# Performance work log

Measured on AMD Instinct MI355X. Metric: run time of the kernel, lower is better.

The kernel has to match this reference:

```python
import jax, jax.numpy as jnp
import numpy as np

N_NODES = 100000
E_MAIN = 1600000   # '_E' edges
E_ACC = 200000     # 'account' edges
D = 128            # dim_in == dim_out
FE = 4             # edge feature width (hard-coded in source)


def setup_inputs() -> dict:
    key = jax.random.key(0)
    ks = jax.random.split(key, 14)
    inp = {
        "feats": jax.random.normal(ks[0], (N_NODES, D), jnp.float32),
        "edge_feats": jax.random.normal(ks[1], (E_MAIN, FE), jnp.float32),
        "src_E": jax.random.randint(ks[2], (E_MAIN,), 0, N_NODES),
        "dst_E": jax.random.randint(ks[3], (E_MAIN,), 0, N_NODES),
        "src_acc": jax.random.randint(ks[4], (E_ACC,), 0, N_NODES),
        "dst_acc": jax.random.randint(ks[5], (E_ACC,), 0, N_NODES),
        "W_skip": jax.random.normal(ks[6], (D, D), jnp.float32) * 0.05,
        "b_skip": jnp.zeros((D,), jnp.float32),
        "W_msg": jax.random.normal(ks[7], (D, D), jnp.float32) * 0.05,
        "b_msg": jnp.zeros((D,), jnp.float32),
        "W_edge": jax.random.normal(ks[8], (D, FE), jnp.float32) * 0.5,
        "b_edge": jax.random.normal(ks[9], (D,), jnp.float32) * 0.1,
        "W_att": jax.random.normal(ks[10], (1, FE), jnp.float32) * 0.5,
        "b_att": jax.random.normal(ks[11], (1,), jnp.float32) * 0.1,
    }
    return inp


def reference(feats, edge_feats, src_E, dst_E, src_acc, dst_acc,
              W_skip, b_skip, W_msg, b_msg, W_edge, b_edge, W_att, b_att):
    n = feats.shape[0]
    # symmetric-ish degree norm from '_E' source rows (matches self.norm)
    deg = jax.ops.segment_sum(jnp.ones(src_E.shape[0], feats.dtype), src_E,
                              num_segments=n)
    deg_safe = jnp.where(deg > 0, deg, 1.0)
    norm = jnp.where(deg > 0, deg_safe ** -0.5, 0.0)  # [N]
    h = feats * norm[:, None]                         # srcdata['h'] == dstdata['h']

    def messages(ef, s, d):
        # per-edge: sigmoid attention * src + transformed edge feat + dst
        att = jax.nn.sigmoid(ef @ W_att.T + b_att)    # [E,1]
        tr = ef @ W_edge.T + b_edge                   # [E,D]
        return att * h[s] + tr + h[d]                 # [E,D]

    agg = jax.ops.segment_sum(messages(edge_feats, src_E, dst_E), dst_E,
                              num_segments=n)
    # 'account' etype gets zero edge features (as in source)
    ef_acc = jnp.zeros((src_acc.shape[0], edge_feats.shape[1]), feats.dtype)
    agg = agg + jax.ops.segment_sum(messages(ef_acc, src_acc, dst_acc), dst_acc,
                                    num_segments=n)

    rst = agg * norm[:, None]
    return rst @ W_msg.T + b_msg + (feats @ W_skip.T + b_skip)
```

## Files before the change

### kernel.cpp

```cpp
#include <hip/hip_runtime.h>
#include <hip/hip_bf16.h>

#define NN 100000
#define NP 100096
#define EM 1600000
#define EA 200000
#define ET (EM + EA)
#define SB 98

#define HC 128
#define CNT_CHUNK 14063
#define DEG_CHUNK 12500
#define PITCHW 25024
#define PITCHB 100096

#define OFF_NORM 0
#define OFF_CNT  (NN)
#define OFF_CUR  (2*NN)
#define OFF_BSUM (3*NN)
#define OFF_WB   (3*NN + 128)
#define OFF_REC  (OFF_WB + 16384)
#define OFF_FB   (OFF_REC + 4*ET)
#define OFF_RB   (OFF_FB + 64*NP)
#define OFF_RANK (OFF_RB + 64*NP)

#define UNP_LO(u) __uint_as_float((u) << 16)
#define UNP_HI(u) __uint_as_float((u) & 0xFFFF0000u)

typedef __attribute__((ext_vector_type(8))) short bf16x8;
typedef __attribute__((ext_vector_type(4))) float f32x4;

static __device__ __forceinline__ unsigned pack_bf16x2(float a, float b) {
  union { __hip_bfloat162 v; unsigned u; } cv;
  cv.v = __float22bfloat162_rn(make_float2(a, b));
  return cv.u;
}

__global__ __launch_bounds__(1024) void k_hist(
    const int* __restrict__ srcE, const int* __restrict__ dstE,
    const int* __restrict__ dstA, const float* __restrict__ feats,
    unsigned* __restrict__ featsb,
    unsigned* __restrict__ hist8w, unsigned* __restrict__ deg8w,
    unsigned short* __restrict__ rank16) {
  __shared__ unsigned h[PITCHW];
  int tid = threadIdx.x;
  int bid = blockIdx.x;

  for (int i = bid * 1024 + tid; i < NP * 64; i += 2 * HC * 1024) {
    if (i < NN * 64) {
      float2 f = ((const float2*)feats)[i];
      featsb[i] = pack_bf16x2(f.x, f.y);
    } else {
      featsb[i] = 0u;
    }
  }

  for (int i = tid; i < PITCHW; i += 1024) h[i] = 0u;
  __syncthreads();
  if (bid < HC) {
    int c = bid;
    int e1 = c * CNT_CHUNK + CNT_CHUNK; if (e1 > ET) e1 = ET;
    for (int e = c * CNT_CHUNK + tid; e < e1; e += 1024) {
      int d = (e < EM) ? dstE[e] : dstA[e - EM];
      unsigned sh = 8u * (unsigned)(d & 3);
      unsigned old = atomicAdd(&h[d >> 2], 1u << sh);
      unsigned lr = (old >> sh) & 255u;
      rank16[e] = (unsigned short)(((unsigned)c << 9) | lr);
    }
    __syncthreads();
    unsigned* dst = hist8w + (size_t)c * PITCHW;
    for (int i = tid; i < PITCHW; i += 1024) dst[i] = h[i];
  } else {
    int c = bid - HC;
    int e1 = c * DEG_CHUNK + DEG_CHUNK;
    for (int e = c * DEG_CHUNK + tid; e < e1; e += 1024) {
      int s = srcE[e];
      atomicAdd(&h[s >> 2], 1u << (8u * (unsigned)(s & 3)));
    }
    __syncthreads();
    unsigned* dst = deg8w + (size_t)c * PITCHW;
    for (int i = tid; i < PITCHW; i += 1024) dst[i] = h[i];
  }
}

__global__ __launch_bounds__(256) void k_merge_wt(
    unsigned char* __restrict__ hist8, const unsigned char* __restrict__ deg8,
    unsigned* __restrict__ cnt, float* __restrict__ norm,
    const float* __restrict__ Wmsg, const float* __restrict__ Wskip,
    unsigned* __restrict__ Wb) {
  int i = blockIdx.x * 256 + threadIdx.x;
  if (i < NN) {
    unsigned t = 0;
    for (int c = 0; c < HC; ++c) {
      unsigned char* p = hist8 + (size_t)c * PITCHB + i;
      unsigned b = *p;
      *p = (unsigned char)t;
      t += b;
    }
    cnt[i] = t;
    unsigned dg = 0;
    for (int c = 0; c < HC; ++c) dg += deg8[(size_t)c * PITCHB + i];
    norm[i] = dg ? rsqrtf((float)dg) : 0.0f;
  }
  if (i < 16384) {
    int j = i >> 7, kk = i & 127;
    float a, b;
    if (kk < 64) {
      a = Wmsg[j * 128 + 2 * kk];
      b = Wmsg[j * 128 + 2 * kk + 1];
    } else {
      a = Wskip[j * 128 + 2 * kk - 128];
      b = Wskip[j * 128 + 2 * kk - 127];
    }
    Wb[j * 128 + kk] = pack_bf16x2(a, b);
  }
}

__global__ __launch_bounds__(1024) void k_scan1(const unsigned* __restrict__ cnt,
                                                int* __restrict__ bsum) {
  __shared__ int ws16[16];
  int tid = threadIdx.x, lane = tid & 63, wid = tid >> 6;
  int i = blockIdx.x * 1024 + tid;
  int v = (i < NN) ? (int)cnt[i] : 0;
#pragma unroll
  for (int s = 1; s < 64; s <<= 1) v += __shfl_xor(v, s, 64);
  if (lane == 0) ws16[wid] = v;
  __syncthreads();
  if (tid == 0) {
    int a = 0;
#pragma unroll
    for (int w = 0; w < 16; ++w) a += ws16[w];
    bsum[blockIdx.x] = a;
  }
}

__global__ __launch_bounds__(64) void k_scan2(int* __restrict__ bsum) {
  int lane = threadIdx.x;
  int v0 = (lane < SB) ? bsum[lane] : 0;
  int v1 = (64 + lane < SB) ? bsum[64 + lane] : 0;
  int x0 = v0, x1 = v1;
#pragma unroll
  for (int s = 1; s < 64; s <<= 1) {
    int y = __shfl_up(x0, s, 64); if (lane >= s) x0 += y;
  }
#pragma unroll
  for (int s = 1; s < 64; s <<= 1) {
    int y = __shfl_up(x1, s, 64); if (lane >= s) x1 += y;
  }
  int t0 = __shfl(x0, 63, 64);
  if (lane < SB) bsum[lane] = x0 - v0;
  if (64 + lane < SB) bsum[64 + lane] = t0 + x1 - v1;
}

__global__ __launch_bounds__(1024) void k_scan3(const unsigned* __restrict__ cnt,
                                                const int* __restrict__ bsum,
                                                int* __restrict__ cursor) {
  __shared__ int ws16[16];
  int tid = threadIdx.x, lane = tid & 63, wid = tid >> 6;
  int i = blockIdx.x * 1024 + tid;
  int v = (i < NN) ? (int)cnt[i] : 0;
  int x = v;
#pragma unroll
  for (int s = 1; s < 64; s <<= 1) {
    int y = __shfl_up(x, s, 64); if (lane >= s) x += y;
  }
  if (lane == 63) ws16[wid] = x;
  __syncthreads();
  if (tid == 0) {
    int a = bsum[blockIdx.x];
#pragma unroll
    for (int w = 0; w < 16; ++w) { int t = ws16[w]; ws16[w] = a; a += t; }
  }
  __syncthreads();
  if (i < NN) cursor[i] = ws16[wid] + x - v;
}

__global__ __launch_bounds__(256) void k_fill(
    const int* __restrict__ srcE, const int* __restrict__ dstE,
    const int* __restrict__ srcA, const int* __restrict__ dstA,
    const float* __restrict__ ef, const float* __restrict__ Watt,
    const float* __restrict__ batt, const float* __restrict__ norm,
    const int* __restrict__ cursor, const unsigned char* __restrict__ hist8,
    const unsigned short* __restrict__ rank16,
    uint4* __restrict__ rec) {
  int e = blockIdx.x * 256 + threadIdx.x;
  if (e >= ET) return;
  int s, d;
  float att;
  float4 f;
  if (e < EM) {
    s = srcE[e]; d = dstE[e];
    f = ((const float4*)ef)[e];
    float z = f.x * Watt[0] + f.y * Watt[1] + f.z * Watt[2] + f.w * Watt[3] + batt[0];
    att = 1.0f / (1.0f + __expf(-z));
  } else {
    int ea = e - EM;
    s = srcA[ea]; d = dstA[ea];
    f = make_float4(0.f, 0.f, 0.f, 0.f);
    att = 1.0f / (1.0f + __expf(-batt[0]));
  }
  float c = att * norm[s];
  unsigned rr = rank16[e];
  int slot = cursor[d] + (int)hist8[(size_t)(rr >> 9) * PITCHB + d]
           + (int)(rr & 511u);
  rec[slot] = make_uint4((unsigned)s, __float_as_uint(c),
                         pack_bf16x2(f.x, f.y), pack_bf16x2(f.z, f.w));
}

__global__ __launch_bounds__(256) void k_pull(
    const float* __restrict__ feats, const unsigned* __restrict__ featsb,
    const unsigned* __restrict__ cnt, const int* __restrict__ cursor,
    const float* __restrict__ norm, const uint4* __restrict__ rec,
    const float* __restrict__ Wedge, const float* __restrict__ bedge,
    unsigned* __restrict__ rstb) {
  int lane = threadIdx.x & 63, wid = threadIdx.x >> 6;
  int n = blockIdx.x * 4 + wid;
  if (n >= NP) return;
  if (n >= NN) { rstb[n * 64 + lane] = 0u; return; }

  int beg = __builtin_amdgcn_readfirstlane(cursor[n]);
  int len = __builtin_amdgcn_readfirstlane((int)cnt[n]);
  int end = beg + len;
  float2 acc = make_float2(0.f, 0.f);
  float4 efa = make_float4(0.f, 0.f, 0.f, 0.f);
  int e = beg;
  for (; e + 8 <= end; e += 8) {
    uint4 r0 = rec[e+0], r1 = rec[e+1], r2 = rec[e+2], r3 = rec[e+3];
    uint4 r4 = rec[e+4], r5 = rec[e+5], r6 = rec[e+6], r7 = rec[e+7];
    unsigned u0 = featsb[r0.x * 64 + lane];
    unsigned u1 = featsb[r1.x * 64 + lane];
    unsigned u2 = featsb[r2.x * 64 + lane];
    unsigned u3 = featsb[r3.x * 64 + lane];
    unsigned u4 = featsb[r4.x * 64 + lane];
    unsigned u5 = featsb[r5.x * 64 + lane];
    unsigned u6 = featsb[r6.x * 64 + lane];
    unsigned u7 = featsb[r7.x * 64 + lane];
    float c0 = __uint_as_float(r0.y), c1 = __uint_as_float(r1.y);
    float c2 = __uint_as_float(r2.y), c3 = __uint_as_float(r3.y);
    float c4 = __uint_as_float(r4.y), c5 = __uint_as_float(r5.y);
    float c6 = __uint_as_float(r6.y), c7 = __uint_as_float(r7.y);
    acc.x += c0 * UNP_LO(u0) + c1 * UNP_LO(u1) + c2 * UNP_LO(u2) + c3 * UNP_LO(u3)
           + c4 * UNP_LO(u4) + c5 * UNP_LO(u5) + c6 * UNP_LO(u6) + c7 * UNP_LO(u7);
    acc.y += c0 * UNP_HI(u0) + c1 * UNP_HI(u1) + c2 * UNP_HI(u2) + c3 * UNP_HI(u3)
           + c4 * UNP_HI(u4) + c5 * UNP_HI(u5) + c6 * UNP_HI(u6) + c7 * UNP_HI(u7);
    efa.x += UNP_LO(r0.z) + UNP_LO(r1.z) + UNP_LO(r2.z) + UNP_LO(r3.z)
           + UNP_LO(r4.z) + UNP_LO(r5.z) + UNP_LO(r6.z) + UNP_LO(r7.z);
    efa.y += UNP_HI(r0.z) + UNP_HI(r1.z) + UNP_HI(r2.z) + UNP_HI(r3.z)
           + UNP_HI(r4.z) + UNP_HI(r5.z) + UNP_HI(r6.z) + UNP_HI(r7.z);
    efa.z += UNP_LO(r0.w) + UNP_LO(r1.w) + UNP_LO(r2.w) + UNP_LO(r3.w)
           + UNP_LO(r4.w) + UNP_LO(r5.w) + UNP_LO(r6.w) + UNP_LO(r7.w);
    efa.w += UNP_HI(r0.w) + UNP_HI(r1.w) + UNP_HI(r2.w) + UNP_HI(r3.w)
           + UNP_HI(r4.w) + UNP_HI(r5.w) + UNP_HI(r6.w) + UNP_HI(r7.w);
  }
  for (; e < end; ++e) {
    uint4 r = rec[e];
    unsigned u = featsb[r.x * 64 + lane];
    float c = __uint_as_float(r.y);
    acc.x += c * UNP_LO(u);
    acc.y += c * UNP_HI(u);
    efa.x += UNP_LO(r.z); efa.y += UNP_HI(r.z);
    efa.z += UNP_LO(r.w); efa.w += UNP_HI(r.w);
  }
  float flen = (float)len;
  float nm = norm[n];
  float2 f = ((const float2*)feats)[n * 64 + lane];
  float4 wa = ((const float4*)Wedge)[2 * lane + 0];
  float4 wb = ((const float4*)Wedge)[2 * lane + 1];
  float2 be = ((const float2*)bedge)[lane];
  float tx = wa.x * efa.x + wa.y * efa.y + wa.z * efa.z + wa.w * efa.w;
  float ty = wb.x * efa.x + wb.y * efa.y + wb.z * efa.z + wb.w * efa.w;
  float rx = (acc.x + tx + flen * (be.x + nm * f.x)) * nm;
  float ry = (acc.y + ty + flen * (be.y + nm * f.y)) * nm;
  rstb[n * 64 + lane] = pack_bf16x2(rx, ry);
}

__global__ __launch_bounds__(256) void k_gemm(
    const unsigned* __restrict__ rstb, const unsigned* __restrict__ featsb,
    const unsigned* __restrict__ Wb,
    const float* __restrict__ bmsg, const float* __restrict__ bskip,
    float* __restrict__ out) {
  int lane = threadIdx.x & 63, wid = threadIdx.x >> 6;
  int quad = lane >> 4, l15 = lane & 15;
  int rowt = blockIdx.x * 128 + wid * 32;
  int m0 = rowt + l15;
  int m1 = m0 + 16;

  f32x4 acc0[8], acc1[8];
#pragma unroll
  for (int ct = 0; ct < 8; ++ct) {
    acc0[ct] = (f32x4){0.f, 0.f, 0.f, 0.f};
    acc1[ct] = (f32x4){0.f, 0.f, 0.f, 0.f};
  }

#pragma unroll
  for (int ks = 0; ks < 8; ++ks) {
    int kb = ks * 32;
    const unsigned* Xsrc = (kb < 128) ? rstb : featsb;
    int off = ((kb & 127) >> 1) + quad * 4;
    bf16x8 a0 = *(const bf16x8*)(Xsrc + m0 * 64 + off);
    bf16x8 a1 = *(const bf16x8*)(Xsrc + m1 * 64 + off);
#pragma unroll
    for (int ct = 0; ct < 8; ++ct) {
      int j = ct * 16 + l15;
      bf16x8 b = *(const bf16x8*)(Wb + j * 128 + (kb >> 1) + quad * 4);
      acc0[ct] = __builtin_amdgcn_mfma_f32_16x16x32_bf16(a0, b, acc0[ct], 0, 0, 0);
      acc1[ct] = __builtin_amdgcn_mfma_f32_16x16x32_bf16(a1, b, acc1[ct], 0, 0, 0);
    }
  }

#pragma unroll
  for (int ct = 0; ct < 8; ++ct) {
    int col = ct * 16 + l15;
    float bia = bmsg[col] + bskip[col];
#pragma unroll
    for (int r = 0; r < 4; ++r) {
      int row0 = rowt + quad * 4 + r;
      if (row0 < NN) out[row0 * 128 + col] = acc0[ct][r] + bia;
      int row1 = row0 + 16;
      if (row1 < NN) out[row1 * 128 + col] = acc1[ct][r] + bia;
    }
  }
}

extern "C" void kernel_launch(void* const* d_in, const int* in_sizes, int n_in,
                              void* d_out, int out_size, void* d_ws, size_t ws_size,
                              hipStream_t stream) {
  const float* feats  = (const float*)d_in[0];
  const float* ef     = (const float*)d_in[1];
  const int*   srcE   = (const int*)d_in[2];
  const int*   dstE   = (const int*)d_in[3];
  const int*   srcA   = (const int*)d_in[4];
  const int*   dstA   = (const int*)d_in[5];
  const float* Wskip  = (const float*)d_in[6];
  const float* bskip  = (const float*)d_in[7];
  const float* Wmsg   = (const float*)d_in[8];
  const float* bmsg   = (const float*)d_in[9];
  const float* Wedge  = (const float*)d_in[10];
  const float* bedge  = (const float*)d_in[11];
  const float* Watt   = (const float*)d_in[12];
  const float* batt   = (const float*)d_in[13];
  float* out = (float*)d_out;
  float* ws  = (float*)d_ws;

  float*          norm   = ws + OFF_NORM;
  unsigned*       cnt    = (unsigned*)(ws + OFF_CNT);
  int*            cursor = (int*)(ws + OFF_CUR);
  int*            bsum   = (int*)(ws + OFF_BSUM);
  unsigned*       Wb     = (unsigned*)(ws + OFF_WB);
  uint4*          rec    = (uint4*)(ws + OFF_REC);
  unsigned*       featsb = (unsigned*)(ws + OFF_FB);
  unsigned*       rstb   = (unsigned*)(ws + OFF_RB);
  unsigned short* rank16 = (unsigned short*)(ws + OFF_RANK);

  unsigned*       hist8w = rstb;
  unsigned*       deg8w  = rstb + (size_t)HC * PITCHW;
  unsigned char*  hist8b = (unsigned char*)hist8w;
  unsigned char*  deg8b  = (unsigned char*)deg8w;

  k_hist<<<2 * HC, 1024, 0, stream>>>(srcE, dstE, dstA, feats, featsb,
                                      hist8w, deg8w, rank16);
  k_merge_wt<<<(NN + 255) / 256, 256, 0, stream>>>(hist8b, deg8b, cnt, norm,
                                                   Wmsg, Wskip, Wb);
  k_scan1<<<SB, 1024, 0, stream>>>(cnt, bsum);
  k_scan2<<<1, 64, 0, stream>>>(bsum);
  k_scan3<<<SB, 1024, 0, stream>>>(cnt, bsum, cursor);
  k_fill<<<(ET + 255) / 256, 256, 0, stream>>>(srcE, dstE, srcA, dstA, ef, Watt,
                                               batt, norm, cursor, hist8b,
                                               rank16, rec);
  k_pull<<<NP / 4, 256, 0, stream>>>(feats, featsb, cnt, cursor, norm,
                                     rec, Wedge, bedge, rstb);
  k_gemm<<<NP / 128, 256, 0, stream>>>(rstb, featsb, Wb, bmsg, bskip, out);
}
```

Baseline: 374.4 us.

## Fuse pull aggregation and output GEMM into one kernel via LDS tile

Merges the per-node gather/aggregate kernel and the MFMA GEMM into a single kernel: each 256-thread block aggregates 64 nodes (16 per wave, sequentially) into a bf16 LDS tile, then runs the GEMM on that tile plus the bf16 features. This removes the global round trip of the intermediate rst buffer and one launch, and reads the destination features from the bf16 copy instead of fp32. The trade-off is fewer blocks (NP/64 instead of NP/4), each wave processing 16 nodes serially, which lowers memory-level parallelism for the latency-bound gather. The self term also loses precision from using bf16 feats.

New measurement: 415.2 us. 10.9% more time.

```diff
diff --git a/kernel.cpp b/kernel.cpp
--- a/kernel.cpp
+++ b/kernel.cpp
@@ -21,8 +21,8 @@
 #define OFF_WB   (3*NN + 128)
 #define OFF_REC  (OFF_WB + 16384)
 #define OFF_FB   (OFF_REC + 4*ET)
-#define OFF_RB   (OFF_FB + 64*NP)
-#define OFF_RANK (OFF_RB + 64*NP)
+#define OFF_HIST (OFF_FB + 64*NP)
+#define OFF_RANK (OFF_HIST + 64*NP)
 
 #define UNP_LO(u) __uint_as_float((u) << 16)
 #define UNP_HI(u) __uint_as_float((u) & 0xFFFF0000u)
@@ -207,104 +207,109 @@
                          pack_bf16x2(f.x, f.y), pack_bf16x2(f.z, f.w));
 }
 
-__global__ __launch_bounds__(256) void k_pull(
-    const float* __restrict__ feats, const unsigned* __restrict__ featsb,
+__global__ __launch_bounds__(256, 4) void k_pullgemm(
+    const unsigned* __restrict__ featsb,
     const unsigned* __restrict__ cnt, const int* __restrict__ cursor,
     const float* __restrict__ norm, const uint4* __restrict__ rec,
     const float* __restrict__ Wedge, const float* __restrict__ bedge,
-    unsigned* __restrict__ rstb) {
+    const unsigned* __restrict__ Wb,
+    const float* __restrict__ bmsg, const float* __restrict__ bskip,
+    float* __restrict__ out) {
+  __shared__ unsigned lA[64 * 68];
   int lane = threadIdx.x & 63, wid = threadIdx.x >> 6;
-  int n = blockIdx.x * 4 + wid;
-  if (n >= NP) return;
-  if (n >= NN) { rstb[n * 64 + lane] = 0u; return; }
-
-  int beg = __builtin_amdgcn_readfirstlane(cursor[n]);
-  int len = __builtin_amdgcn_readfirstlane((int)cnt[n]);
-  int end = beg + len;
-  float2 acc = make_float2(0.f, 0.f);
-  float4 efa = make_float4(0.f, 0.f, 0.f, 0.f);
-  int e = beg;
-  for (; e + 8 <= end; e += 8) {
-    uint4 r0 = rec[e+0], r1 = rec[e+1], r2 = rec[e+2], r3 = rec[e+3];
-    uint4 r4 = rec[e+4], r5 = rec[e+5], r6 = rec[e+6], r7 = rec[e+7];
-    unsigned u0 = featsb[r0.x * 64 + lane];
-    unsigned u1 = featsb[r1.x * 64 + lane];
-    unsigned u2 = featsb[r2.x * 64 + lane];
-    unsigned u3 = featsb[r3.x * 64 + lane];
-    unsigned u4 = featsb[r4.x * 64 + lane];
-    unsigned u5 = featsb[r5.x * 64 + lane];
-    unsigned u6 = featsb[r6.x * 64 + lane];
-    unsigned u7 = featsb[r7.x * 64 + lane];
-    float c0 = __uint_as_float(r0.y), c1 = __uint_as_float(r1.y);
-    float c2 = __uint_as_float(r2.y), c3 = __uint_as_float(r3.y);
-    float c4 = __uint_as_float(r4.y), c5 = __uint_as_float(r5.y);
-    float c6 = __uint_as_float(r6.y), c7 = __uint_as_float(r7.y);
-    acc.x += c0 * UNP_LO(u0) + c1 * UNP_LO(u1) + c2 * UNP_LO(u2) + c3 * UNP_LO(u3)
-           + c4 * UNP_LO(u4) + c5 * UNP_LO(u5) + c6 * UNP_LO(u6) + c7 * UNP_LO(u7);
-    acc.y += c0 * UNP_HI(u0) + c1 * UNP_HI(u1) + c2 * UNP_HI(u2) + c3 * UNP_HI(u3)
-           + c4 * UNP_HI(u4) + c5 * UNP_HI(u5) + c6 * UNP_HI(u6) + c7 * UNP_HI(u7);
-    efa.x += UNP_LO(r0.z) + UNP_LO(r1.z) + UNP_LO(r2.z) + UNP_LO(r3.z)
-           + UNP_LO(r4.z) + UNP_LO(r5.z) + UNP_LO(r6.z) + UNP_LO(r7.z);
-    efa.y += UNP_HI(r0.z) + UNP_HI(r1.z) + UNP_HI(r2.z) + UNP_HI(r3.z)
-           + UNP_HI(r4.z) + UNP_HI(r5.z) + UNP_HI(r6.z) + UNP_HI(r7.z);
-    efa.z += UNP_LO(r0.w) + UNP_LO(r1.w) + UNP_LO(r2.w) + UNP_LO(r3.w)
-           + UNP_LO(r4.w) + UNP_LO(r5.w) + UNP_LO(r6.w) + UNP_LO(r7.w);
-    efa.w += UNP_HI(r0.w) + UNP_HI(r1.w) + UNP_HI(r2.w) + UNP_HI(r3.w)
-           + UNP_HI(r4.w) + UNP_HI(r5.w) + UNP_HI(r6.w) + UNP_HI(r7.w);
-  }
-  for (; e < end; ++e) {
-    uint4 r = rec[e];
-    unsigned u = featsb[r.x * 64 + lane];
-    float c = __uint_as_float(r.y);
-    acc.x += c * UNP_LO(u);
-    acc.y += c * UNP_HI(u);
-    efa.x += UNP_LO(r.z); efa.y += UNP_HI(r.z);
-    efa.z += UNP_LO(r.w); efa.w += UNP_HI(r.w);
-  }
-  float flen = (float)len;
-  float nm = norm[n];
-  float2 f = ((const float2*)feats)[n * 64 + lane];
+  int rowt = blockIdx.x * 64;
+
   float4 wa = ((const float4*)Wedge)[2 * lane + 0];
   float4 wb = ((const float4*)Wedge)[2 * lane + 1];
   float2 be = ((const float2*)bedge)[lane];
-  float tx = wa.x * efa.x + wa.y * efa.y + wa.z * efa.z + wa.w * efa.w;
-  float ty = wb.x * efa.x + wb.y * efa.y + wb.z * efa.z + wb.w * efa.w;
-  float rx = (acc.x + tx + flen * (be.x + nm * f.x)) * nm;
-  float ry = (acc.y + ty + flen * (be.y + nm * f.y)) * nm;
-  rstb[n * 64 + lane] = pack_bf16x2(rx, ry);
-}
-
-__global__ __launch_bounds__(256) void k_gemm(
-    const unsigned* __restrict__ rstb, const unsigned* __restrict__ featsb,
-    const unsigned* __restrict__ Wb,
-    const float* __restrict__ bmsg, const float* __restrict__ bskip,
-    float* __restrict__ out) {
-  int lane = threadIdx.x & 63, wid = threadIdx.x >> 6;
+
+  for (int i = 0; i < 16; ++i) {
+    int rloc = wid * 16 + i;
+    int n = rowt + rloc;
+    float rx = 0.f, ry = 0.f;
+    if (n < NN) {
+      int beg = __builtin_amdgcn_readfirstlane(cursor[n]);
+      int len = __builtin_amdgcn_readfirstlane((int)cnt[n]);
+      int end = beg + len;
+      float2 acc = make_float2(0.f, 0.f);
+      float4 efa = make_float4(0.f, 0.f, 0.f, 0.f);
+      int e = beg;
+      for (; e + 8 <= end; e += 8) {
+        uint4 r0 = rec[e+0], r1 = rec[e+1], r2 = rec[e+2], r3 = rec[e+3];
+        uint4 r4 = rec[e+4], r5 = rec[e+5], r6 = rec[e+6], r7 = rec[e+7];
+        unsigned u0 = featsb[r0.x * 64 + lane];
+        unsigned u1 = featsb[r1.x * 64 + lane];
+        unsigned u2 = featsb[r2.x * 64 + lane];
+        unsigned u3 = featsb[r3.x * 64 + lane];
+        unsigned u4 = featsb[r4.x * 64 + lane];
+        unsigned u5 = featsb[r5.x * 64 + lane];
+        unsigned u6 = featsb[r6.x * 64 + lane];
+        unsigned u7 = featsb[r7.x * 64 + lane];
+        float c0 = __uint_as_float(r0.y), c1 = __uint_as_float(r1.y);
+        float c2 = __uint_as_float(r2.y), c3 = __uint_as_float(r3.y);
+        float c4 = __uint_as_float(r4.y), c5 = __uint_as_float(r5.y);
+        float c6 = __uint_as_float(r6.y), c7 = __uint_as_float(r7.y);
+        acc.x += c0 * UNP_LO(u0) + c1 * UNP_LO(u1) + c2 * UNP_LO(u2)
+               + c3 * UNP_LO(u3) + c4 * UNP_LO(u4) + c5 * UNP_LO(u5)
+               + c6 * UNP_LO(u6) + c7 * UNP_LO(u7);
+        acc.y += c0 * UNP_HI(u0) + c1 * UNP_HI(u1) + c2 * UNP_HI(u2)
+               + c3 * UNP_HI(u3) + c4 * UNP_HI(u4) + c5 * UNP_HI(u5)
+               + c6 * UNP_HI(u6) + c7 * UNP_HI(u7);
+        efa.x += UNP_LO(r0.z) + UNP_LO(r1.z) + UNP_LO(r2.z) + UNP_LO(r3.z)
+               + UNP_LO(r4.z) + UNP_LO(r5.z) + UNP_LO(r6.z) + UNP_LO(r7.z);
+        efa.y += UNP_HI(r0.z) + UNP_HI(r1.z) + UNP_HI(r2.z) + UNP_HI(r3.z)
+               + UNP_HI(r4.z) + UNP_HI(r5.z) + UNP_HI(r6.z) + UNP_HI(r7.z);
+        efa.z += UNP_LO(r0.w) + UNP_LO(r1.w) + UNP_LO(r2.w) + UNP_LO(r3.w)
+               + UNP_LO(r4.w) + UNP_LO(r5.w) + UNP_LO(r6.w) + UNP_LO(r7.w);
+        efa.w += UNP_HI(r0.w) + UNP_HI(r1.w) + UNP_HI(r2.w) + UNP_HI(r3.w)
+               + UNP_HI(r4.w) + UNP_HI(r5.w) + UNP_HI(r6.w) + UNP_HI(r7.w);
+      }
+      for (; e < end; ++e) {
+        uint4 r = rec[e];
+        unsigned u = featsb[r.x * 64 + lane];
+        float c = __uint_as_float(r.y);
+        acc.x += c * UNP_LO(u);
+        acc.y += c * UNP_HI(u);
+        efa.x += UNP_LO(r.z); efa.y += UNP_HI(r.z);
+        efa.z += UNP_LO(r.w); efa.w += UNP_HI(r.w);
+      }
+      float flen = (float)len;
+      float nm = norm[n];
+      unsigned ud = featsb[n * 64 + lane];
+      float fx = UNP_LO(ud), fy = UNP_HI(ud);
+      float tx = wa.x * efa.x + wa.y * efa.y + wa.z * efa.z + wa.w * efa.w;
+      float ty = wb.x * efa.x + wb.y * efa.y + wb.z * efa.z + wb.w * efa.w;
+      rx = (acc.x + tx + flen * (be.x + nm * fx)) * nm;
+      ry = (acc.y + ty + flen * (be.y + nm * fy)) * nm;
+    }
+    lA[rloc * 68 + lane] = pack_bf16x2(rx, ry);
+  }
+  __syncthreads();
+
   int quad = lane >> 4, l15 = lane & 15;
-  int rowt = blockIdx.x * 128 + wid * 32;
-  int m0 = rowt + l15;
-  int m1 = m0 + 16;
-
-  f32x4 acc0[8], acc1[8];
-#pragma unroll
-  for (int ct = 0; ct < 8; ++ct) {
-    acc0[ct] = (f32x4){0.f, 0.f, 0.f, 0.f};
-    acc1[ct] = (f32x4){0.f, 0.f, 0.f, 0.f};
-  }
+  int rloc0 = wid * 16 + l15;
+  int m0 = rowt + rloc0;
+
+  f32x4 acc0[8];
+#pragma unroll
+  for (int ct = 0; ct < 8; ++ct) acc0[ct] = (f32x4){0.f, 0.f, 0.f, 0.f};
 
 #pragma unroll
   for (int ks = 0; ks < 8; ++ks) {
     int kb = ks * 32;
-    const unsigned* Xsrc = (kb < 128) ? rstb : featsb;
-    int off = ((kb & 127) >> 1) + quad * 4;
-    bf16x8 a0 = *(const bf16x8*)(Xsrc + m0 * 64 + off);
-    bf16x8 a1 = *(const bf16x8*)(Xsrc + m1 * 64 + off);
+    bf16x8 a0;
+    if (ks < 4) {
+      int off = ks * 16 + quad * 4;
+      a0 = *(const bf16x8*)(&lA[rloc0 * 68 + off]);
+    } else {
+      int off = ((kb & 127) >> 1) + quad * 4;
+      a0 = *(const bf16x8*)(featsb + (size_t)m0 * 64 + off);
+    }
 #pragma unroll
     for (int ct = 0; ct < 8; ++ct) {
       int j = ct * 16 + l15;
       bf16x8 b = *(const bf16x8*)(Wb + j * 128 + (kb >> 1) + quad * 4);
       acc0[ct] = __builtin_amdgcn_mfma_f32_16x16x32_bf16(a0, b, acc0[ct], 0, 0, 0);
-      acc1[ct] = __builtin_amdgcn_mfma_f32_16x16x32_bf16(a1, b, acc1[ct], 0, 0, 0);
     }
   }
 
@@ -314,10 +319,8 @@
     float bia = bmsg[col] + bskip[col];
 #pragma unroll
     for (int r = 0; r < 4; ++r) {
-      int row0 = rowt + quad * 4 + r;
+      int row0 = rowt + wid * 16 + quad * 4 + r;
       if (row0 < NN) out[row0 * 128 + col] = acc0[ct][r] + bia;
-      int row1 = row0 + 16;
-      if (row1 < NN) out[row1 * 128 + col] = acc1[ct][r] + bia;
     }
   }
 }
@@ -349,11 +352,10 @@
   unsigned*       Wb     = (unsigned*)(ws + OFF_WB);
   uint4*          rec    = (uint4*)(ws + OFF_REC);
   unsigned*       featsb = (unsigned*)(ws + OFF_FB);
-  unsigned*       rstb   = (unsigned*)(ws + OFF_RB);
   unsigned short* rank16 = (unsigned short*)(ws + OFF_RANK);
 
-  unsigned*       hist8w = rstb;
-  unsigned*       deg8w  = rstb + (size_t)HC * PITCHW;
+  unsigned*       hist8w = (unsigned*)(ws + OFF_HIST);
+  unsigned*       deg8w  = hist8w + (size_t)HC * PITCHW;
   unsigned char*  hist8b = (unsigned char*)hist8w;
   unsigned char*  deg8b  = (unsigned char*)deg8w;
 
@@ -367,7 +369,6 @@
   k_fill<<<(ET + 255) / 256, 256, 0, stream>>>(srcE, dstE, srcA, dstA, ef, Watt,
                                                batt, norm, cursor, hist8b,
                                                rank16, rec);
-  k_pull<<<NP / 4, 256, 0, stream>>>(feats, featsb, cnt, cursor, norm,
-                                     rec, Wedge, bedge, rstb);
-  k_gemm<<<NP / 128, 256, 0, stream>>>(rstb, featsb, Wb, bmsg, bskip, out);
-}
+  k_pullgemm<<<NP / 64, 256, 0, stream>>>(featsb, cnt, cursor, norm, rec,
+                                          Wedge, bedge, Wb, bmsg, bskip, out);
+}
```

## Merge packed byte histograms per word and fuse block-sum scan into merge

Applied to the files above, without the earlier changes.

The merge kernel now processes four nodes per thread. It reads the 8-bit histograms as 32-bit words and does the per-byte exclusive prefix with packed word adds. It also computes the per-block totals, so the separate k_scan1 launch is removed. k_pull now reads the bf16 copy of feats for the dst self term instead of the fp32 array, which cuts bandwidth but lowers precision. The packed adds assume per-node counts stay below 256, and the merge now runs only 98 blocks, so occupancy drops.

Result: no change. 370.0 us (-1.2%).

```diff
diff --git a/kernel.cpp b/kernel.cpp
--- a/kernel.cpp
+++ b/kernel.cpp
@@ -84,24 +84,46 @@
 }
 
 __global__ __launch_bounds__(256) void k_merge_wt(
-    unsigned char* __restrict__ hist8, const unsigned char* __restrict__ deg8,
+    unsigned* __restrict__ hist8w, const unsigned* __restrict__ deg8w,
     unsigned* __restrict__ cnt, float* __restrict__ norm,
+    int* __restrict__ bsum,
     const float* __restrict__ Wmsg, const float* __restrict__ Wskip,
     unsigned* __restrict__ Wb) {
-  int i = blockIdx.x * 256 + threadIdx.x;
-  if (i < NN) {
-    unsigned t = 0;
+  __shared__ int ws4[4];
+  int tid = threadIdx.x;
+  int i = blockIdx.x * 256 + tid;
+  int tot = 0;
+  if (i < PITCHW) {
+    unsigned t4 = 0;
+#pragma unroll 16
     for (int c = 0; c < HC; ++c) {
-      unsigned char* p = hist8 + (size_t)c * PITCHB + i;
-      unsigned b = *p;
-      *p = (unsigned char)t;
-      t += b;
-    }
-    cnt[i] = t;
-    unsigned dg = 0;
-    for (int c = 0; c < HC; ++c) dg += deg8[(size_t)c * PITCHB + i];
-    norm[i] = dg ? rsqrtf((float)dg) : 0.0f;
-  }
+      unsigned* p = hist8w + (size_t)c * PITCHW + i;
+      unsigned w = *p;
+      *p = t4;
+      t4 += w;
+    }
+    unsigned d4 = 0;
+#pragma unroll 16
+    for (int c = 0; c < HC; ++c) d4 += deg8w[(size_t)c * PITCHW + i];
+    int n0 = i * 4;
+#pragma unroll
+    for (int k = 0; k < 4; ++k) {
+      unsigned b = (t4 >> (8 * k)) & 255u;
+      tot += (int)b;
+      if (n0 + k < NN) {
+        cnt[n0 + k] = b;
+        unsigned dg = (d4 >> (8 * k)) & 255u;
+        norm[n0 + k] = dg ? rsqrtf((float)dg) : 0.0f;
+      }
+    }
+  }
+  int lane = tid & 63, wid = tid >> 6;
+#pragma unroll
+  for (int s = 1; s < 64; s <<= 1) tot += __shfl_xor(tot, s, 64);
+  if (lane == 0) ws4[wid] = tot;
+  __syncthreads();
+  if (tid == 0) bsum[blockIdx.x] = ws4[0] + ws4[1] + ws4[2] + ws4[3];
+
   if (i < 16384) {
     int j = i >> 7, kk = i & 127;
     float a, b;
@@ -113,24 +135,6 @@
       b = Wskip[j * 128 + 2 * kk - 127];
     }
     Wb[j * 128 + kk] = pack_bf16x2(a, b);
-  }
-}
-
-__global__ __launch_bounds__(1024) void k_scan1(const unsigned* __restrict__ cnt,
-                                                int* __restrict__ bsum) {
-  __shared__ int ws16[16];
-  int tid = threadIdx.x, lane = tid & 63, wid = tid >> 6;
-  int i = blockIdx.x * 1024 + tid;
-  int v = (i < NN) ? (int)cnt[i] : 0;
-#pragma unroll
-  for (int s = 1; s < 64; s <<= 1) v += __shfl_xor(v, s, 64);
-  if (lane == 0) ws16[wid] = v;
-  __syncthreads();
-  if (tid == 0) {
-    int a = 0;
-#pragma unroll
-    for (int w = 0; w < 16; ++w) a += ws16[w];
-    bsum[blockIdx.x] = a;
   }
 }
 
@@ -208,7 +212,7 @@
 }
 
 __global__ __launch_bounds__(256) void k_pull(
-    const float* __restrict__ feats, const unsigned* __restrict__ featsb,
+    const unsigned* __restrict__ featsb,
     const unsigned* __restrict__ cnt, const int* __restrict__ cursor,
     const float* __restrict__ norm, const uint4* __restrict__ rec,
     const float* __restrict__ Wedge, const float* __restrict__ bedge,
@@ -263,14 +267,15 @@
   }
   float flen = (float)len;
   float nm = norm[n];
-  float2 f = ((const float2*)feats)[n * 64 + lane];
+  unsigned ud = featsb[n * 64 + lane];
+  float fx = UNP_LO(ud), fy = UNP_HI(ud);
   float4 wa = ((const float4*)Wedge)[2 * lane + 0];
   float4 wb = ((const float4*)Wedge)[2 * lane + 1];
   float2 be = ((const float2*)bedge)[lane];
   float tx = wa.x * efa.x + wa.y * efa.y + wa.z * efa.z + wa.w * efa.w;
   float ty = wb.x * efa.x + wb.y * efa.y + wb.z * efa.z + wb.w * efa.w;
-  float rx = (acc.x + tx + flen * (be.x + nm * f.x)) * nm;
-  float ry = (acc.y + ty + flen * (be.y + nm * f.y)) * nm;
+  float rx = (acc.x + tx + flen * (be.x + nm * fx)) * nm;
+  float ry = (acc.y + ty + flen * (be.y + nm * fy)) * nm;
   rstb[n * 64 + lane] = pack_bf16x2(rx, ry);
 }
 
@@ -355,19 +360,17 @@
   unsigned*       hist8w = rstb;
   unsigned*       deg8w  = rstb + (size_t)HC * PITCHW;
   unsigned char*  hist8b = (unsigned char*)hist8w;
-  unsigned char*  deg8b  = (unsigned char*)deg8w;
 
   k_hist<<<2 * HC, 1024, 0, stream>>>(srcE, dstE, dstA, feats, featsb,
                                       hist8w, deg8w, rank16);
-  k_merge_wt<<<(NN + 255) / 256, 256, 0, stream>>>(hist8b, deg8b, cnt, norm,
-                                                   Wmsg, Wskip, Wb);
-  k_scan1<<<SB, 1024, 0, stream>>>(cnt, bsum);
+  k_merge_wt<<<SB, 256, 0, stream>>>(hist8w, deg8w, cnt, norm, bsum,
+                                     Wmsg, Wskip, Wb);
   k_scan2<<<1, 64, 0, stream>>>(bsum);
   k_scan3<<<SB, 1024, 0, stream>>>(cnt, bsum, cursor);
   k_fill<<<(ET + 255) / 256, 256, 0, stream>>>(srcE, dstE, srcA, dstA, ef, Watt,
                                                batt, norm, cursor, hist8b,
                                                rank16, rec);
-  k_pull<<<NP / 4, 256, 0, stream>>>(feats, featsb, cnt, cursor, norm,
+  k_pull<<<NP / 4, 256, 0, stream>>>(featsb, cnt, cursor, norm,
                                      rec, Wedge, bedge, rstb);
   k_gemm<<<NP / 128, 256, 0, stream>>>(rstb, featsb, Wb, bmsg, bskip, out);
 }
```
